# Performance work log

Measured on AMD Instinct MI355X. Metric: run time of the kernel, lower is better.

The kernel has to match this reference:

```python
import jax, jax.numpy as jnp
import numpy as np

B, N, NSAMPLE = 8, 2048, 32
D = 64          # input feature channels
C1, C2 = 64, 128  # MLP channels (channels list after +3 on input: 67 -> 64 -> 128)
RADIUS = 0.15
EPS = 1e-5


def setup_inputs() -> dict:
    key = jax.random.key(0)
    ks = jax.random.split(key, 4)
    position = jax.random.uniform(ks[0], (B, N, 3), dtype=jnp.float32)
    feature = jax.random.normal(ks[1], (B, N, D), dtype=jnp.float32)
    W1 = jax.random.normal(ks[2], (D + 3, C1), dtype=jnp.float32) * 0.05
    gamma1 = jnp.ones((C1,), jnp.float32)
    beta1 = jnp.zeros((C1,), jnp.float32)
    W2 = jax.random.normal(ks[3], (C1, C2), dtype=jnp.float32) * 0.05
    gamma2 = jnp.ones((C2,), jnp.float32)
    beta2 = jnp.zeros((C2,), jnp.float32)
    return {"position": position, "feature": feature,
            "W1": W1, "gamma1": gamma1, "beta1": beta1,
            "W2": W2, "gamma2": gamma2, "beta2": beta2}


def _ball_query(xyz, radius, nsample):
    # squared pairwise distances [B, N, N]
    sq = (jnp.sum(xyz ** 2, -1)[:, :, None]
          + jnp.sum(xyz ** 2, -1)[:, None, :]
          - 2.0 * jnp.einsum('bnc,bmc->bnm', xyz, xyz))
    n = xyz.shape[1]
    idx = jnp.where(sq > radius ** 2, n, jnp.arange(n, dtype=jnp.int32)[None, None, :])
    idx = jnp.sort(idx, axis=-1)[:, :, :nsample]            # [B, N, nsample]
    first = idx[:, :, :1]
    return jnp.where(idx == n, first, idx)                  # pad misses with first neighbor


def _gather(points, idx):
    # points [B, N, C], idx [B, S, K] -> [B, S, K, C]
    b, s, k = idx.shape
    flat = jnp.take_along_axis(points, idx.reshape(b, s * k, 1), axis=1)
    return flat.reshape(b, s, k, points.shape[-1])


def _bn_relu(x, gamma, beta, relu=True):
    # BatchNorm1d over channel dim (train-mode stats across B*N*S), per linearblock
    mean = jnp.mean(x, axis=(0, 1, 2), keepdims=True)
    var = jnp.var(x, axis=(0, 1, 2), keepdims=True)
    y = (x - mean) * jax.lax.rsqrt(var + EPS) * gamma + beta
    return jax.nn.relu(y) if relu else y


def reference(position, feature, W1, gamma1, beta1, W2, gamma2, beta2):
    b, n, _ = position.shape
    idx = _ball_query(position, RADIUS, NSAMPLE)            # [B, N, nsample]
    grouped_xyz = _gather(position, idx) - position[:, :, None, :]  # [B,N,ns,3]
    grouped_feat = _gather(feature, idx)                    # [B, N, ns, D]
    h = jnp.concatenate([grouped_xyz, grouped_feat], axis=-1)  # [B, N, ns, 3+D]
    h = _bn_relu(h @ W1, gamma1, beta1)                     # [B, N, ns, C1]
    h = _bn_relu(h @ W2, gamma2, beta2)                     # [B, N, ns, C2]
    new_feature = jnp.max(h, axis=2)                        # [B, N, C2]
    return position, new_feature
```

## Files before the change

### kernel.cpp

```cpp
#include <hip/hip_runtime.h>
#include <hip/hip_bf16.h>


#define BB 8
#define NN 2048
#define KK 32
#define DD 64
#define CC1 64
#define CC2 128
#define TOTROWS (BB*NN*KK)
#define SITES (BB*NN)
#define PSLICES 256

typedef __bf16 bf16x8 __attribute__((ext_vector_type(8)));
typedef float  f32x4  __attribute__((ext_vector_type(4)));

__device__ __forceinline__ void lds_add(float* p, float v) {
  __hip_atomic_fetch_add(p, v, __ATOMIC_RELAXED, __HIP_MEMORY_SCOPE_WORKGROUP);
}

__global__ __launch_bounds__(256) void k1_ball(const float* __restrict__ pos,
                                               int* __restrict__ idx)
{
  __shared__ float4 P[NN];
  const int b = blockIdx.x >> 6;
  const int qbase = (blockIdx.x & 63) * 32;
  for (int i = threadIdx.x; i < NN; i += 256) {
    const float* p = pos + ((size_t)b*NN + i)*3;
    float x = p[0], y = p[1], z = p[2];
    float s = __fadd_rn(__fadd_rn(__fmul_rn(x,x), __fmul_rn(y,y)), __fmul_rn(z,z));
    P[i] = make_float4(x, y, z, s);
  }
  __syncthreads();
  const int wave = threadIdx.x >> 6, lane = threadIdx.x & 63;
  const float R2 = (float)(0.15 * 0.15);
  const unsigned long long lt = (lane == 63) ? 0x7fffffffffffffffull
                                             : ((1ull << lane) - 1ull);
  for (int qi = wave; qi < 32; qi += 4) {
    const int q = qbase + qi;
    const float4 Q = P[q];
    int* ip = idx + ((size_t)b*NN + q)*KK;
    int cnt = 0, first = -1;
    for (int step = 0; step < 32; ++step) {
      float4 p = P[step*64 + lane];
      float d = __fmul_rn(Q.x, p.x);
      d = fmaf(Q.y, p.y, d);
      d = fmaf(Q.z, p.z, d);
      float sq = __fsub_rn(__fadd_rn(Q.w, p.w), __fmul_rn(2.0f, d));
      bool in = !(sq > R2);
      unsigned long long mask = __ballot(in);
      if (first < 0 && mask) first = step*64 + (int)__builtin_ctzll(mask);
      int dst = cnt + (int)__popcll(mask & lt);
      if (in && dst < KK) ip[dst] = step*64 + lane;
      cnt += (int)__popcll(mask);
      if (cnt >= KK) break;
    }
    if (lane >= cnt && lane < KK) ip[lane] = first;
  }
}

__global__ __launch_bounds__(1024, 1) void kP_scatter(
    const float* __restrict__ pos, const int* __restrict__ idx,
    float* __restrict__ Pc, float* __restrict__ Px,
    float* __restrict__ Py, float* __restrict__ Pz,
    float* __restrict__ mom)
{
  __shared__ unsigned int Sc[NN], Sx[NN], Sy[NN], Sz[NN];
  __shared__ float mred[16*9];
  const int b = blockIdx.x >> 5;
  const int slice = blockIdx.x & 31;
  for (int i = threadIdx.x; i < NN; i += 1024) {
    Sc[i] = 0u; Sx[i] = 0u; Sy[i] = 0u; Sz[i] = 0u;
  }
  __syncthreads();
  const float* pb = pos + (size_t)b*NN*3;
  const int sl = threadIdx.x >> 4;
  const int kg = threadIdx.x & 15;
  const int site = slice*64 + sl;
  const int* ip = idx + ((size_t)(b*NN + site))*KK;
  const int ip0 = ip[0];
  const float cx = pb[site*3], cy = pb[site*3+1], cz = pb[site*3+2];
  const float FS = 4194304.0f;
  float m1x=0.f,m1y=0.f,m1z=0.f,mxx=0.f,myy=0.f,mzz=0.f,mxy=0.f,mxz=0.f,myz=0.f;
  int wt = 0;
  #pragma unroll
  for (int j = 0; j < 2; ++j) {
    const int k = kg*2 + j;
    const int m = ip[k];
    float dx = pb[m*3  ] - cx;
    float dy = pb[m*3+1] - cy;
    float dz = pb[m*3+2] - cz;
    if (k > 0 && m == ip0) {
      ++wt;
    } else {
      atomicAdd(&Sc[m], 1u);
      atomicAdd(&Sx[m], (unsigned int)__float2int_rn(dx*FS));
      atomicAdd(&Sy[m], (unsigned int)__float2int_rn(dy*FS));
      atomicAdd(&Sz[m], (unsigned int)__float2int_rn(dz*FS));
    }
    m1x += dx; m1y += dy; m1z += dz;
    mxx = fmaf(dx,dx,mxx); myy = fmaf(dy,dy,myy); mzz = fmaf(dz,dz,mzz);
    mxy = fmaf(dx,dy,mxy); mxz = fmaf(dx,dz,mxz); myz = fmaf(dy,dz,myz);
  }
  if (wt > 0) {
    float dx0 = pb[ip0*3  ] - cx;
    float dy0 = pb[ip0*3+1] - cy;
    float dz0 = pb[ip0*3+2] - cz;
    atomicAdd(&Sc[ip0], (unsigned int)wt);
    atomicAdd(&Sx[ip0], (unsigned int)(wt*__float2int_rn(dx0*FS)));
    atomicAdd(&Sy[ip0], (unsigned int)(wt*__float2int_rn(dy0*FS)));
    atomicAdd(&Sz[ip0], (unsigned int)(wt*__float2int_rn(dz0*FS)));
  }
  const int lane = threadIdx.x & 63;
  const int wv = threadIdx.x >> 6;
  float vals[9] = {m1x,m1y,m1z,mxx,myy,mzz,mxy,mxz,myz};
  #pragma unroll
  for (int i = 0; i < 9; ++i) {
    float v = vals[i];
    #pragma unroll
    for (int s = 1; s < 64; s <<= 1) v += __shfl_xor(v, s, 64);
    if (lane == 0) mred[wv*9 + i] = v;
  }
  __syncthreads();
  const float IS = 2.38418579101562500e-7f;
  float* pc = Pc + (size_t)blockIdx.x*NN;
  float* px = Px + (size_t)blockIdx.x*NN;
  float* py = Py + (size_t)blockIdx.x*NN;
  float* pz = Pz + (size_t)blockIdx.x*NN;
  for (int i = threadIdx.x; i < NN; i += 1024) {
    pc[i] = (float)Sc[i];
    px[i] = (float)(int)Sx[i] * IS;
    py[i] = (float)(int)Sy[i] * IS;
    pz[i] = (float)(int)Sz[i] * IS;
  }
  if (threadIdx.x < 9) {
    float s = 0.f;
    #pragma unroll
    for (int w2 = 0; w2 < 16; ++w2) s += mred[w2*9 + threadIdx.x];
    unsafeAtomicAdd(&mom[threadIdx.x], s);
  }
}

__global__ __launch_bounds__(256) void kR_reduce(
    const float* __restrict__ Pc, const float* __restrict__ Px,
    const float* __restrict__ Py, const float* __restrict__ Pz,
    float* __restrict__ cnt, float* __restrict__ DXa,
    float* __restrict__ DYa, float* __restrict__ DZa)
{
  int i = blockIdx.x*256 + threadIdx.x;
  int a = i >> 14;
  int j = i & 16383;
  int b = j >> 11, m = j & (NN-1);
  const float* P = (a == 0) ? Pc : (a == 1) ? Px : (a == 2) ? Py : Pz;
  float s = 0.f;
  #pragma unroll
  for (int sl = 0; sl < 32; ++sl) s += P[(size_t)(b*32 + sl)*NN + m];
  float* O = (a == 0) ? cnt : (a == 1) ? DXa : (a == 2) ? DYa : DZa;
  O[j] = s;
}

__global__ __launch_bounds__(256) void kB_g(const float* __restrict__ feat,
                                            const float* __restrict__ W1,
                                            const float* __restrict__ cnt,
                                            const float* __restrict__ DXa,
                                            const float* __restrict__ DYa,
                                            const float* __restrict__ DZa,
                                            float* __restrict__ g,
                                            float* __restrict__ A)
{
  __shared__ float red[320];
  for (int i = threadIdx.x; i < 320; i += 256) red[i] = 0.f;
  __syncthreads();
  const int lane = threadIdx.x & 63;
  const int quad = lane >> 4;
  const int col  = lane & 15;
  const int gw = (blockIdx.x*256 + threadIdx.x) >> 6;

  bf16x8 Bf[2][4];
  #pragma unroll
  for (int kt = 0; kt < 2; ++kt)
    #pragma unroll
    for (int nt = 0; nt < 4; ++nt) {
      bf16x8 v;
      #pragma unroll
      for (int j = 0; j < 8; ++j)
        v[j] = (__bf16)W1[(3 + kt*32 + quad*8 + j)*CC1 + nt*16 + col];
      Bf[kt][nt] = v;
    }
  float a1[4], a2[4], a3[4], a4[4], a5[4];
  #pragma unroll
  for (int nt = 0; nt < 4; ++nt) { a1[nt]=0.f; a2[nt]=0.f; a3[nt]=0.f; a4[nt]=0.f; a5[nt]=0.f; }

  for (int t = 0; t < 2; ++t) {
    const int row0 = (gw*2 + t) * 16;
    bf16x8 Af[2];
    #pragma unroll
    for (int kt = 0; kt < 2; ++kt) {
      const float4* fp =
        (const float4*)(feat + (size_t)(row0 + col)*DD + kt*32 + quad*8);
      float4 f0 = fp[0], f1 = fp[1];
      float fv[8] = {f0.x,f0.y,f0.z,f0.w,f1.x,f1.y,f1.z,f1.w};
      bf16x8 v;
      #pragma unroll
      for (int j = 0; j < 8; ++j) v[j] = (__bf16)fv[j];
      Af[kt] = v;
    }
    float cw[4], dxw[4], dyw[4], dzw[4];
    #pragma unroll
    for (int r = 0; r < 4; ++r) {
      int row = row0 + quad*4 + r;
      cw[r] = cnt[row]; dxw[r] = DXa[row]; dyw[r] = DYa[row]; dzw[r] = DZa[row];
    }
    #pragma unroll
    for (int nt = 0; nt < 4; ++nt) {
      f32x4 a = {0.f, 0.f, 0.f, 0.f};
      a = __builtin_amdgcn_mfma_f32_16x16x32_bf16(Af[0], Bf[0][nt], a, 0, 0, 0);
      a = __builtin_amdgcn_mfma_f32_16x16x32_bf16(Af[1], Bf[1][nt], a, 0, 0, 0);
      #pragma unroll
      for (int r = 0; r < 4; ++r) {
        float v = a[r];
        g[(size_t)(row0 + quad*4 + r)*CC1 + nt*16 + col] = v;
        float cv = cw[r]*v;
        a1[nt] += cv; a2[nt] = fmaf(cv, v, a2[nt]);
        a3[nt] = fmaf(dxw[r], v, a3[nt]);
        a4[nt] = fmaf(dyw[r], v, a4[nt]);
        a5[nt] = fmaf(dzw[r], v, a5[nt]);
      }
    }
  }
  #pragma unroll
  for (int nt = 0; nt < 4; ++nt) {
    float v1=a1[nt], v2=a2[nt], v3=a3[nt], v4=a4[nt], v5=a5[nt];
    v1 += __shfl_xor(v1,16,64); v1 += __shfl_xor(v1,32,64);
    v2 += __shfl_xor(v2,16,64); v2 += __shfl_xor(v2,32,64);
    v3 += __shfl_xor(v3,16,64); v3 += __shfl_xor(v3,32,64);
    v4 += __shfl_xor(v4,16,64); v4 += __shfl_xor(v4,32,64);
    v5 += __shfl_xor(v5,16,64); v5 += __shfl_xor(v5,32,64);
    if (quad == 0) {
      int ch = nt*16 + col;
      lds_add(&red[ch], v1);
      lds_add(&red[64+ch], v2);
      lds_add(&red[128+ch], v3);
      lds_add(&red[192+ch], v4);
      lds_add(&red[256+ch], v5);
    }
  }
  __syncthreads();
  for (int i = threadIdx.x; i < 320; i += 256) unsafeAtomicAdd(&A[i], red[i]);
}

__global__ __launch_bounds__(256) void kS_fold(
    const float* __restrict__ W1, const float* __restrict__ gamma1,
    const float* __restrict__ beta1, const float* __restrict__ A,
    const float* __restrict__ mom,
    float* __restrict__ sc1, float* __restrict__ sh1, float* __restrict__ W1s)
{
  int c = threadIdx.x;
  if (c >= CC1) return;
  float wx = W1[c], wy = W1[CC1+c], wz = W1[2*CC1+c];
  float A1 = A[c], A2 = A[64+c], A3x = A[128+c], A3y = A[192+c], A3z = A[256+c];
  float sum1 = A1 + wx*mom[0] + wy*mom[1] + wz*mom[2];
  float ss = A2 + 2.f*(wx*A3x + wy*A3y + wz*A3z)
           + wx*wx*mom[3] + wy*wy*mom[4] + wz*wz*mom[5]
           + 2.f*(wx*wy*mom[6] + wx*wz*mom[7] + wy*wz*mom[8]);
  const float invN = 1.0f / (float)TOTROWS;
  float mean = sum1 * invN;
  float var  = ss * invN - mean*mean;
  float sc = rsqrtf(var + 1e-5f) * gamma1[c];
  float sh = beta1[c] - mean * sc;
  sc1[c] = sc; sh1[c] = sh;
  W1s[c] = wx*sc; W1s[64+c] = wy*sc; W1s[128+c] = wz*sc;
}

__global__ __launch_bounds__(256, 2) void kD_mfma(
    const float* __restrict__ pos, const int* __restrict__ idx,
    const float* __restrict__ g, const float* __restrict__ sc1,
    const float* __restrict__ sh1, const float* __restrict__ W1s,
    const float* __restrict__ W2,
    float* __restrict__ stats2, float* __restrict__ out_nf)
{
  __shared__ float red2[256];
  red2[threadIdx.x] = 0.f;
  __syncthreads();
  const int lane = threadIdx.x & 63;
  const int quad = lane >> 4;
  const int col  = lane & 15;
  const int gw = (blockIdx.x*256 + threadIdx.x) >> 6;

  bf16x8 Bf[2][8];
  #pragma unroll
  for (int kt = 0; kt < 2; ++kt)
    #pragma unroll
    for (int nt = 0; nt < 8; ++nt) {
      bf16x8 v;
      #pragma unroll
      for (int j = 0; j < 8; ++j)
        v[j] = (__bf16)W2[(kt*32 + quad*8 + j)*CC2 + nt*16 + col];
      Bf[kt][nt] = v;
    }
  float wxs[2][8], wys[2][8], wzs[2][8], scj[2][8], shj[2][8];
  #pragma unroll
  for (int kt = 0; kt < 2; ++kt)
    #pragma unroll
    for (int j = 0; j < 8; ++j) {
      int c = kt*32 + quad*8 + j;
      wxs[kt][j] = W1s[c]; wys[kt][j] = W1s[64+c]; wzs[kt][j] = W1s[128+c];
      scj[kt][j] = sc1[c]; shj[kt][j] = sh1[c];
    }
  float ssum[8], ssq[8];
  #pragma unroll
  for (int nt = 0; nt < 8; ++nt) { ssum[nt] = 0.f; ssq[nt] = 0.f; }

  for (int si = 0; si < 4; ++si) {
    const int site = gw*4 + si;
    const int b = site >> 11;
    const float* pc = pos + (size_t)site*3;
    const float cx = pc[0], cy = pc[1], cz = pc[2];
    int mm[2]; float dx[2], dy[2], dz[2];
    #pragma unroll
    for (int mt = 0; mt < 2; ++mt) {
      mm[mt] = idx[site*KK + mt*16 + col];
      const float* pm = pos + ((size_t)b*NN + mm[mt])*3;
      dx[mt] = pm[0]-cx; dy[mt] = pm[1]-cy; dz[mt] = pm[2]-cz;
    }
    bf16x8 Af[2][2];
    #pragma unroll
    for (int mt = 0; mt < 2; ++mt)
      #pragma unroll
      for (int kt = 0; kt < 2; ++kt) {
        const float4* gp =
          (const float4*)(g + (((size_t)b*NN + mm[mt])*CC1 + kt*32 + quad*8));
        float4 g0 = gp[0], g1 = gp[1];
        float hv[8] = {g0.x,g0.y,g0.z,g0.w,g1.x,g1.y,g1.z,g1.w};
        bf16x8 v;
        #pragma unroll
        for (int j = 0; j < 8; ++j) {
          float t = fmaf(dz[mt], wzs[kt][j],
                    fmaf(dy[mt], wys[kt][j],
                    fmaf(dx[mt], wxs[kt][j], shj[kt][j])));
          float h = fmaf(hv[j], scj[kt][j], t);
          v[j] = (__bf16)fmaxf(h, 0.f);
        }
        Af[mt][kt] = v;
      }
    float mx[8];
    #pragma unroll
    for (int nt = 0; nt < 8; ++nt) mx[nt] = -3.0e38f;
    #pragma unroll
    for (int mt = 0; mt < 2; ++mt) {
      f32x4 acc[8];
      #pragma unroll
      for (int nt = 0; nt < 8; ++nt) {
        f32x4 a = {0.f, 0.f, 0.f, 0.f};
        a = __builtin_amdgcn_mfma_f32_16x16x32_bf16(Af[mt][0], Bf[0][nt], a, 0, 0, 0);
        a = __builtin_amdgcn_mfma_f32_16x16x32_bf16(Af[mt][1], Bf[1][nt], a, 0, 0, 0);
        acc[nt] = a;
      }
      #pragma unroll
      for (int nt = 0; nt < 8; ++nt)
        #pragma unroll
        for (int r = 0; r < 4; ++r) {
          float v = acc[nt][r];
          ssum[nt] += v; ssq[nt] = fmaf(v, v, ssq[nt]);
          mx[nt] = fmaxf(mx[nt], v);
        }
    }
    #pragma unroll
    for (int nt = 0; nt < 8; ++nt) {
      float m = mx[nt];
      m = fmaxf(m, __shfl_xor(m, 16, 64));
      m = fmaxf(m, __shfl_xor(m, 32, 64));
      if ((nt & 3) == quad)
        out_nf[(size_t)site*CC2 + nt*16 + col] = m;
    }
  }
  #pragma unroll
  for (int nt = 0; nt < 8; ++nt) {
    float s = ssum[nt];
    s += __shfl_xor(s, 16, 64); s += __shfl_xor(s, 32, 64);
    float q = ssq[nt];
    q += __shfl_xor(q, 16, 64); q += __shfl_xor(q, 32, 64);
    if (lane < 16) {
      atomicAdd(&red2[nt*16 + col], s);
      atomicAdd(&red2[128 + nt*16 + col], q);
    }
  }
  __syncthreads();
  unsafeAtomicAdd(&stats2[threadIdx.x], red2[threadIdx.x]);
}

__global__ __launch_bounds__(256) void k45_epi(const float* __restrict__ pos,
                                               const float* __restrict__ g2,
                                               const float* __restrict__ be2,
                                               const float* __restrict__ stats2,
                                               float* __restrict__ out)
{
  int i = blockIdx.x*256 + threadIdx.x;
  if (blockIdx.x < 192) { out[i] = pos[i]; return; }
  int j = i - 192*256;
  int c = j & (CC2-1);
  const float invc = 1.0f / (float)TOTROWS;
  float mean = stats2[c] * invc;
  float var  = stats2[128 + c] * invc - mean*mean;
  float sc = rsqrtf(var + 1e-5f) * g2[c];
  float sh = be2[c] - mean * sc;
  float* out_nf = out + (size_t)BB*NN*3;
  float x = out_nf[j];
  out_nf[j] = fmaxf(fmaf(x, sc, sh), 0.f);
}

extern "C" void kernel_launch(void* const* d_in, const int* in_sizes, int n_in,
                              void* d_out, int out_size, void* d_ws, size_t ws_size,
                              hipStream_t stream) {
  const float* pos  = (const float*)d_in[0];
  const float* feat = (const float*)d_in[1];
  const float* W1   = (const float*)d_in[2];
  const float* g1   = (const float*)d_in[3];
  const float* be1  = (const float*)d_in[4];
  const float* W2   = (const float*)d_in[5];
  const float* g2   = (const float*)d_in[6];
  const float* be2  = (const float*)d_in[7];
  float* out = (float*)d_out;
  float* out_nf = out + (size_t)BB*NN*3;

  char* w = (char*)d_ws;
  int*   idx    = (int*)w;
  float* A      = (float*)(w + 0x200000);
  float* mom    = A + 320;
  float* stats2 = mom + 16;
  float* sc1    = stats2 + 256;
  float* sh1    = sc1 + 64;
  float* W1s    = sh1 + 64;
  float* cnt    = (float*)(w + 0x210000);
  float* DXa    = cnt + SITES;
  float* DYa    = DXa + SITES;
  float* DZa    = DYa + SITES;
  float* Pc     = (float*)(w + 0x260000);
  float* Px     = Pc + (size_t)PSLICES*NN;
  float* Py     = Px + (size_t)PSLICES*NN;
  float* Pz     = Py + (size_t)PSLICES*NN;
  float* g      = (float*)(w + 0x260000);

  hipMemsetAsync(A, 0, (320 + 16 + 256)*sizeof(float), stream);
  k1_ball   <<<512, 256, 0, stream>>>(pos, idx);
  kP_scatter<<<256, 1024, 0, stream>>>(pos, idx, Pc, Px, Py, Pz, mom);
  kR_reduce <<<256, 256, 0, stream>>>(Pc, Px, Py, Pz, cnt, DXa, DYa, DZa);
  kB_g      <<<128, 256, 0, stream>>>(feat, W1, cnt, DXa, DYa, DZa, g, A);
  kS_fold   <<<1, 256, 0, stream>>>(W1, g1, be1, A, mom, sc1, sh1, W1s);
  kD_mfma   <<<1024, 256, 0, stream>>>(pos, idx, g, sc1, sh1, W1s, W2,
                                       stats2, out_nf);
  k45_epi   <<<192 + (SITES*CC2)/256, 256, 0, stream>>>(pos, g2, be2, stats2, out);
}
```

Before: 195.3 us.

## Stage W2 in LDS as bf16, prefetch indices, and raise occupancy in MFMA kernel

The MFMA layer-2 kernel now stores W2 in shared memory as transposed bf16 once per block and reads the B fragments from LDS per tile, instead of keeping all 16 B fragments in registers. Register pressure drops, so launch bounds go from 2 to 3 waves per SIMD. All neighbor indices for the four sites are loaded up front, the W1/BN parameters use vector loads, and the site loop is fully unrolled with setprio around the MFMA section. The cost is extra LDS reads per tile and a transpose pass at block start.

New measurement: 259.0 us. 1.33x slower.

```diff
diff --git a/kernel.cpp b/kernel.cpp
--- a/kernel.cpp
+++ b/kernel.cpp
@@ -272,107 +272,116 @@
   W1s[c] = wx*sc; W1s[64+c] = wy*sc; W1s[128+c] = wz*sc;
 }
 
-__global__ __launch_bounds__(256, 2) void kD_mfma(
+__global__ __launch_bounds__(256, 3) void kD_mfma(
     const float* __restrict__ pos, const int* __restrict__ idx,
     const float* __restrict__ g, const float* __restrict__ sc1,
     const float* __restrict__ sh1, const float* __restrict__ W1s,
     const float* __restrict__ W2,
     float* __restrict__ stats2, float* __restrict__ out_nf)
 {
+  __shared__ __bf16 W2T[128*72];
   __shared__ float red2[256];
   red2[threadIdx.x] = 0.f;
-  __syncthreads();
+  for (int i = threadIdx.x; i < CC1*CC2; i += 256) {
+    int k = i >> 7, n = i & 127;
+    W2T[n*72 + k] = (__bf16)W2[i];
+  }
+  __syncthreads();
+
   const int lane = threadIdx.x & 63;
   const int quad = lane >> 4;
   const int col  = lane & 15;
   const int gw = (blockIdx.x*256 + threadIdx.x) >> 6;
 
-  bf16x8 Bf[2][8];
-  #pragma unroll
-  for (int kt = 0; kt < 2; ++kt)
+  float wxs[2][8], wys[2][8], wzs[2][8], scj[2][8], shj[2][8];
+  #pragma unroll
+  for (int kt = 0; kt < 2; ++kt) {
+    const int c0 = kt*32 + quad*8;
+    f32x4 x0 = *(const f32x4*)&W1s[c0],       x1 = *(const f32x4*)&W1s[c0+4];
+    f32x4 y0 = *(const f32x4*)&W1s[64+c0],    y1 = *(const f32x4*)&W1s[64+c0+4];
+    f32x4 z0 = *(const f32x4*)&W1s[128+c0],   z1 = *(const f32x4*)&W1s[128+c0+4];
+    f32x4 s0 = *(const f32x4*)&sc1[c0],       s1 = *(const f32x4*)&sc1[c0+4];
+    f32x4 h0 = *(const f32x4*)&sh1[c0],       h1 = *(const f32x4*)&sh1[c0+4];
+    #pragma unroll
+    for (int j = 0; j < 4; ++j) {
+      wxs[kt][j] = x0[j]; wxs[kt][4+j] = x1[j];
+      wys[kt][j] = y0[j]; wys[kt][4+j] = y1[j];
+      wzs[kt][j] = z0[j]; wzs[kt][4+j] = z1[j];
+      scj[kt][j] = s0[j]; scj[kt][4+j] = s1[j];
+      shj[kt][j] = h0[j]; shj[kt][4+j] = h1[j];
+    }
+  }
+
+  int mm[4][2];
+  #pragma unroll
+  for (int si = 0; si < 4; ++si) {
+    #pragma unroll
+    for (int mt = 0; mt < 2; ++mt)
+      mm[si][mt] = idx[(size_t)(gw*4 + si)*KK + mt*16 + col];
+  }
+
+  float ssum[8], ssq[8];
+  #pragma unroll
+  for (int nt = 0; nt < 8; ++nt) { ssum[nt] = 0.f; ssq[nt] = 0.f; }
+
+  #pragma unroll
+  for (int si = 0; si < 4; ++si) {
+    const int site = __builtin_amdgcn_readfirstlane(gw*4 + si);
+    const int b = site >> 11;
+    const float cx = pos[(size_t)site*3];
+    const float cy = pos[(size_t)site*3+1];
+    const float cz = pos[(size_t)site*3+2];
+    bf16x8 Af[2][2];
+    #pragma unroll
+    for (int mt = 0; mt < 2; ++mt) {
+      const int m = mm[si][mt];
+      const float* pm = pos + ((size_t)b*NN + m)*3;
+      const float dx = pm[0]-cx, dy = pm[1]-cy, dz = pm[2]-cz;
+      const float* gr = g + ((size_t)b*NN + m)*CC1 + quad*8;
+      f32x4 ga = *(const f32x4*)gr,        gb = *(const f32x4*)(gr+4);
+      f32x4 gc = *(const f32x4*)(gr+32),   gd = *(const f32x4*)(gr+36);
+      float hv0[8] = {ga.x,ga.y,ga.z,ga.w,gb.x,gb.y,gb.z,gb.w};
+      float hv1[8] = {gc.x,gc.y,gc.z,gc.w,gd.x,gd.y,gd.z,gd.w};
+      bf16x8 v0, v1;
+      #pragma unroll
+      for (int j = 0; j < 8; ++j) {
+        float t0 = fmaf(dz, wzs[0][j],
+                   fmaf(dy, wys[0][j],
+                   fmaf(dx, wxs[0][j], shj[0][j])));
+        float h0 = fmaf(hv0[j], scj[0][j], t0);
+        v0[j] = (__bf16)fmaxf(h0, 0.f);
+        float t1 = fmaf(dz, wzs[1][j],
+                   fmaf(dy, wys[1][j],
+                   fmaf(dx, wxs[1][j], shj[1][j])));
+        float h1 = fmaf(hv1[j], scj[1][j], t1);
+        v1[j] = (__bf16)fmaxf(h1, 0.f);
+      }
+      Af[mt][0] = v0; Af[mt][1] = v1;
+    }
+    __builtin_amdgcn_s_setprio(1);
     #pragma unroll
     for (int nt = 0; nt < 8; ++nt) {
-      bf16x8 v;
+      const bf16x8 B0 = *(const bf16x8*)&W2T[(nt*16 + col)*72 + quad*8];
+      const bf16x8 B1 = *(const bf16x8*)&W2T[(nt*16 + col)*72 + 32 + quad*8];
+      float mxv = -3.0e38f;
       #pragma unroll
-      for (int j = 0; j < 8; ++j)
-        v[j] = (__bf16)W2[(kt*32 + quad*8 + j)*CC2 + nt*16 + col];
-      Bf[kt][nt] = v;
-    }
-  float wxs[2][8], wys[2][8], wzs[2][8], scj[2][8], shj[2][8];
-  #pragma unroll
-  for (int kt = 0; kt < 2; ++kt)
-    #pragma unroll
-    for (int j = 0; j < 8; ++j) {
-      int c = kt*32 + quad*8 + j;
-      wxs[kt][j] = W1s[c]; wys[kt][j] = W1s[64+c]; wzs[kt][j] = W1s[128+c];
-      scj[kt][j] = sc1[c]; shj[kt][j] = sh1[c];
-    }
-  float ssum[8], ssq[8];
-  #pragma unroll
-  for (int nt = 0; nt < 8; ++nt) { ssum[nt] = 0.f; ssq[nt] = 0.f; }
-
-  for (int si = 0; si < 4; ++si) {
-    const int site = gw*4 + si;
-    const int b = site >> 11;
-    const float* pc = pos + (size_t)site*3;
-    const float cx = pc[0], cy = pc[1], cz = pc[2];
-    int mm[2]; float dx[2], dy[2], dz[2];
-    #pragma unroll
-    for (int mt = 0; mt < 2; ++mt) {
-      mm[mt] = idx[site*KK + mt*16 + col];
-      const float* pm = pos + ((size_t)b*NN + mm[mt])*3;
-      dx[mt] = pm[0]-cx; dy[mt] = pm[1]-cy; dz[mt] = pm[2]-cz;
-    }
-    bf16x8 Af[2][2];
-    #pragma unroll
-    for (int mt = 0; mt < 2; ++mt)
-      #pragma unroll
-      for (int kt = 0; kt < 2; ++kt) {
-        const float4* gp =
-          (const float4*)(g + (((size_t)b*NN + mm[mt])*CC1 + kt*32 + quad*8));
-        float4 g0 = gp[0], g1 = gp[1];
-        float hv[8] = {g0.x,g0.y,g0.z,g0.w,g1.x,g1.y,g1.z,g1.w};
-        bf16x8 v;
-        #pragma unroll
-        for (int j = 0; j < 8; ++j) {
-          float t = fmaf(dz[mt], wzs[kt][j],
-                    fmaf(dy[mt], wys[kt][j],
-                    fmaf(dx[mt], wxs[kt][j], shj[kt][j])));
-          float h = fmaf(hv[j], scj[kt][j], t);
-          v[j] = (__bf16)fmaxf(h, 0.f);
-        }
-        Af[mt][kt] = v;
-      }
-    float mx[8];
-    #pragma unroll
-    for (int nt = 0; nt < 8; ++nt) mx[nt] = -3.0e38f;
-    #pragma unroll
-    for (int mt = 0; mt < 2; ++mt) {
-      f32x4 acc[8];
-      #pragma unroll
-      for (int nt = 0; nt < 8; ++nt) {
+      for (int mt = 0; mt < 2; ++mt) {
         f32x4 a = {0.f, 0.f, 0.f, 0.f};
-        a = __builtin_amdgcn_mfma_f32_16x16x32_bf16(Af[mt][0], Bf[0][nt], a, 0, 0, 0);
-        a = __builtin_amdgcn_mfma_f32_16x16x32_bf16(Af[mt][1], Bf[1][nt], a, 0, 0, 0);
-        acc[nt] = a;
-      }
-      #pragma unroll
-      for (int nt = 0; nt < 8; ++nt)
+        a = __builtin_amdgcn_mfma_f32_16x16x32_bf16(Af[mt][0], B0, a, 0, 0, 0);
+        a = __builtin_amdgcn_mfma_f32_16x16x32_bf16(Af[mt][1], B1, a, 0, 0, 0);
         #pragma unroll
         for (int r = 0; r < 4; ++r) {
-          float v = acc[nt][r];
+          float v = a[r];
           ssum[nt] += v; ssq[nt] = fmaf(v, v, ssq[nt]);
-          mx[nt] = fmaxf(mx[nt], v);
+          mxv = fmaxf(mxv, v);
         }
-    }
-    #pragma unroll
-    for (int nt = 0; nt < 8; ++nt) {
-      float m = mx[nt];
-      m = fmaxf(m, __shfl_xor(m, 16, 64));
-      m = fmaxf(m, __shfl_xor(m, 32, 64));
+      }
+      mxv = fmaxf(mxv, __shfl_xor(mxv, 16, 64));
+      mxv = fmaxf(mxv, __shfl_xor(mxv, 32, 64));
       if ((nt & 3) == quad)
-        out_nf[(size_t)site*CC2 + nt*16 + col] = m;
-    }
+        out_nf[(size_t)site*CC2 + nt*16 + col] = mxv;
+    }
+    __builtin_amdgcn_s_setprio(0);
   }
   #pragma unroll
   for (int nt = 0; nt < 8; ++nt) {
```
